# Optimization experiments

Hardware: AMD Instinct MI355X
Metric: run time of the kernel (lower is better)

## Reference

```python
import jax, jax.numpy as jnp
import numpy as np

N_NODES = 65536
N_FEAT = 64
N_EDGES = 1048576
N_GRAPHS = 16
LP_ITERS = 30


def setup_inputs() -> dict:
    key = jax.random.key(0)
    k1, k2, k3 = jax.random.split(key, 3)
    x = jax.random.normal(k1, (N_NODES, N_FEAT), dtype=jnp.float32)
    edge_index = jax.random.randint(k2, (2, N_EDGES), 0, N_NODES, dtype=jnp.int32)
    batch = jnp.sort(jax.random.randint(k3, (N_NODES,), 0, N_GRAPHS, dtype=jnp.int32))
    v2 = jnp.full((1,), 3.5, dtype=jnp.float32)  # learnable affinity scale param
    return {"x": x, "edge_index": edge_index, "batch": batch, "v2": v2}


def _lp_clustering(row, col, aff, n_nodes, n_iters):
    """Label propagation: each node adopts the neighbor label with max summed affinity."""
    E = row.shape[0]
    aff = jax.lax.stop_gradient(aff)  # clustering is discrete, no grad path

    def body(_, labels):
        lab_c = labels[col]                                    # neighbor labels per edge
        order = jnp.lexsort((lab_c, row))                      # sort by (row, neighbor-label)
        r_s, l_s, w_s = row[order], lab_c[order], aff[order]
        new_grp = jnp.concatenate([jnp.ones((1,), bool),
                                   (r_s[1:] != r_s[:-1]) | (l_s[1:] != l_s[:-1])])
        gid = jnp.cumsum(new_grp) - 1                          # dense (row,label) group ids
        gsum = jax.ops.segment_sum(w_s, gid, num_segments=E)   # affinity mass per group
        gcnt = jax.ops.segment_sum(jnp.ones_like(w_s), gid, num_segments=E)
        valid = gcnt > 0
        g_row = jnp.where(valid, jax.ops.segment_max(r_s, gid, num_segments=E), 0)
        g_lab = jnp.where(valid, jax.ops.segment_max(l_s, gid, num_segments=E), n_nodes)
        node_max = jax.ops.segment_max(jnp.where(valid, gsum, -jnp.inf), g_row,
                                       num_segments=n_nodes)
        win = valid & (gsum == node_max[g_row])
        # smallest winning label == torch argmax first-hit tie-break
        return jax.ops.segment_min(jnp.where(win, g_lab, n_nodes), g_row,
                                   num_segments=n_nodes)

    labels0 = jnp.arange(n_nodes, dtype=row.dtype)
    return jax.lax.fori_loop(0, n_iters, body, labels0)


def _forward(x, edge_index, batch, v2):
    n = x.shape[0]
    loops = jnp.arange(n, dtype=edge_index.dtype)
    ei = jnp.concatenate([edge_index, jnp.stack([loops, loops])], axis=1)  # add_self_loops
    row, col = ei[0], ei[1]

    # P2-style affinities: log_aff = -v2 * ||x_i - x_j||^2 ; forward exponentiates
    sqdist = jnp.sum((x[row] - x[col]) ** 2, axis=1)  # [E]
    losses = jnp.mean(sqdist)
    aff = jnp.exp(-v2[0] * sqdist)

    node_labels = _lp_clustering(row, col, aff, n, LP_ITERS)

    # unique(return_inverse): dense relabel of surviving cluster ids (sorted order)
    present = jnp.zeros((n,), jnp.int32).at[node_labels].set(1)
    cluster_labels = (jnp.cumsum(present) - 1)[node_labels]

    # max_pool_x: scatter-max node features into clusters (padded to n rows)
    cx = jax.ops.segment_max(x, cluster_labels, num_segments=n)
    cb = jax.ops.segment_max(batch, cluster_labels, num_segments=n)
    nonempty = jax.ops.segment_sum(jnp.ones((n,), jnp.int32), cluster_labels,
                                   num_segments=n) > 0
    cx = jnp.where(nonempty[:, None], cx, 0.0)
    cb = jnp.where(nonempty, cb, -1)

    # coalesce(cluster_labels[edge_index]): sort + dedupe, duplicates padded with -1
    mr, mc = cluster_labels[row], cluster_labels[col]
    order = jnp.lexsort((mc, mr))
    mr_s, mc_s = mr[order], mc[order]
    dup = jnp.concatenate([jnp.zeros((1,), bool),
                           (mr_s[1:] == mr_s[:-1]) & (mc_s[1:] == mc_s[:-1])])
    cei = jnp.stack([jnp.where(dup, -1, mr_s), jnp.where(dup, -1, mc_s)])

    return cx, cei, cb, cluster_labels, losses


def reference(x, edge_index, batch, v2):
    return _forward(x, edge_index, batch, v2)
```

## Files before the change

### kernel.cpp

```cpp
#include <hip/hip_runtime.h>
#include <hip/hip_fp16.h>
#include <hip/hip_cooperative_groups.h>

namespace cg = cooperative_groups;

#define DI __device__ __forceinline__

constexpr int NN   = 65536;
constexpr int NF   = 64;
constexpr int E0c  = 1048576;
constexpr int ET   = E0c + NN;
constexpr int LPITERS = 30;
constexpr int KPOS = 16;
constexpr int MSCH = 4096;
constexpr int NCHK = ET / MSCH;
constexpr int SCAP = 8192;
constexpr int CAP0 = 6144;
constexpr int EPB  = 128;
constexpr int BPB  = CAP0 / EPB;
constexpr int NPART2 = 256 * BPB;

constexpr int O_CX   = 0;
constexpr int O_CEI0 = NN * NF;
constexpr int O_CEI1 = O_CEI0 + ET;
constexpr int O_CB   = O_CEI0 + 2 * ET;
constexpr int O_CL   = O_CB + NN;
constexpr int O_LOSS = O_CL + NN;

constexpr int W_CHG   = 0;
constexpr int W_NCLUS = 32;
constexpr int W_H1    = 64;
constexpr int W_GC0   = W_H1 + 256;
constexpr int W_GC1   = W_GC0 + 256;
constexpr int W_SCP   = 832;
constexpr int W_SCO   = W_SCP + 256;
constexpr int W_PART  = W_SCO + 256;
constexpr int W_PCNT  = W_PART + NPART2;
constexpr int W_PCOL  = W_PCNT + NN;
constexpr int W_PW    = W_PCOL + NN*KPOS;
constexpr int W_L0    = W_PW + NN*KPOS;
constexpr int W_L1    = W_L0 + NN;
constexpr int W_PRES  = W_L1 + NN;
constexpr int W_PSUM  = W_PRES + NN;
constexpr int W_CLU   = W_PSUM + NN;
constexpr int W_CBA   = W_CLU + NN;
constexpr int W_K0    = W_CBA + NN;
constexpr int W_K1    = W_K0 + 256*CAP0;

DI void edge_rc(const int* ei, int e, int& r, int& c) {
  if (e < E0c) { r = ei[e]; c = ei[E0c + e]; }
  else         { r = e - E0c; c = r; }
}

DI unsigned fenc(float f) {
  unsigned u = __float_as_uint(f);
  return (u & 0x80000000u) ? ~u : (u | 0x80000000u);
}
DI float fdec(unsigned u) {
  u = (u & 0x80000000u) ? (u & 0x7fffffffu) : ~u;
  return __uint_as_float(u);
}

DI int lp_step(int r, int d, int c0, int c1, float q0, float q1,
               const int* __restrict__ pcol, const float* __restrict__ pw,
               const int* __restrict__ lin) {
  int bl = NN;
  if (d == 1) {
    bl = lin[c0];
  } else if (d == 2) {
    int l0 = lin[c0], l1 = lin[c1];
    if (l0 == l1) bl = l0;
    else if (q1 > q0 || (q1 == q0 && l1 < l0)) bl = l1;
    else bl = l0;
  } else if (d > 2) {
    float best = 0.f;
    for (int i = 0; i < d; ++i) {
      int li = lin[pcol[r * KPOS + i]];
      bool dup = false;
      for (int j = 0; j < i; ++j)
        if (lin[pcol[r * KPOS + j]] == li) { dup = true; break; }
      if (dup) continue;
      float sum = 0.f;
      for (int j = i; j < d; ++j)
        if (lin[pcol[r * KPOS + j]] == li) sum += pw[r * KPOS + j];
      if (sum > best || (sum == best && li < bl)) { best = sum; bl = li; }
    }
  }
  return bl;
}


__global__ __launch_bounds__(256) void init_small(int* ws) {
  for (int i = threadIdx.x; i < 832; i += 256) ws[i] = 0;
}

__global__ __launch_bounds__(256) void emultisplit(const int* __restrict__ ei,
                                                   int* __restrict__ gcur0,
                                                   unsigned* __restrict__ K0,
                                                   int* __restrict__ pcnt,
                                                   int* __restrict__ L0,
                                                   const float2* __restrict__ x2,
                                                   unsigned* __restrict__ xh) {
  __shared__ unsigned skey[MSCH];
  __shared__ unsigned short binid[MSCH];
  __shared__ int hl[256], ss[256], hs[256], hc[256], gb[256];
  int t = threadIdx.x;
  if (blockIdx.x < 256) {
    int rr = blockIdx.x * 256 + t;
    pcnt[rr] = 0;
    L0[rr] = rr;
  }
  for (int i = blockIdx.x * 256 + t; i < NN * NF / 2; i += NCHK * 256) {
    float2 f = x2[i];
    __half2 h = __floats2half2_rn(f.x, f.y);
    xh[i] = *reinterpret_cast<unsigned*>(&h);
  }
  hl[t] = 0; __syncthreads();
  int base = blockIdx.x * MSCH;
  unsigned mykey[MSCH / 256];
  #pragma unroll
  for (int k = 0; k < MSCH / 256; ++k) {
    int e = base + k * 256 + t;
    int r, c; edge_rc(ei, e, r, c);
    unsigned key = ((unsigned)r << 16) | (unsigned)c;
    mykey[k] = key;
    atomicAdd(&hl[key >> 24], 1);
  }
  __syncthreads();
  int v = hl[t];
  ss[t] = v; __syncthreads();
  for (int off = 1; off < 256; off <<= 1) {
    int u = (t >= off) ? ss[t - off] : 0;
    __syncthreads();
    ss[t] += u;
    __syncthreads();
  }
  int excl = ss[t] - v;
  hs[t] = excl;
  hc[t] = excl;
  gb[t] = t * CAP0 + ((v > 0) ? atomicAdd(&gcur0[t], v) : 0);
  for (int j = excl; j < excl + v; ++j) binid[j] = (unsigned short)t;
  __syncthreads();
  #pragma unroll
  for (int k = 0; k < MSCH / 256; ++k) {
    int b = mykey[k] >> 24;
    int slot = atomicAdd(&hc[b], 1);
    skey[slot] = mykey[k];
  }
  __syncthreads();
  for (int i = t; i < MSCH; i += 256) {
    int b = binid[i];
    int pos = gb[b] + (i - hs[b]);
    if (pos < (b + 1) * CAP0) K0[pos] = skey[i];
  }
}

__global__ __launch_bounds__(256, 1) void edge_pos2(
    const unsigned* __restrict__ xh, const unsigned* __restrict__ K0,
    const int* __restrict__ gcur0, const float* __restrict__ v2,
    float* __restrict__ part, int* __restrict__ pcnt,
    int* __restrict__ pcol, float* __restrict__ pw) {
  __shared__ float ls[32];
  int t = threadIdx.x, grp = t >> 3, lane = t & 7;
  int bkt = blockIdx.x / BPB;
  int off = (blockIdx.x % BPB) * EPB;
  int cnt = gcur0[bkt];
  if (off >= cnt) {
    if (t == 0) part[blockIdx.x] = 0.f;
    return;
  }
  float w = v2[0];
  unsigned kk[4]; bool act[4];
  uint4 A[4], B[4];
  #pragma unroll
  for (int q = 0; q < 4; ++q) {
    int j = off + grp * 4 + q;
    act[q] = (j < cnt);
    kk[q] = K0[bkt * CAP0 + (act[q] ? j : 0)];
  }
  #pragma unroll
  for (int q = 0; q < 4; ++q) {
    int r = kk[q] >> 16, c = kk[q] & 0xFFFF;
    A[q] = ((const uint4*)(xh + (size_t)r * 32))[lane];
    B[q] = ((const uint4*)(xh + (size_t)c * 32))[lane];
  }
  __builtin_amdgcn_sched_barrier(0);
  float lsum = 0.f;
  #pragma unroll
  for (int q = 0; q < 4; ++q) {
    const __half2* ah = reinterpret_cast<const __half2*>(&A[q]);
    const __half2* bh = reinterpret_cast<const __half2*>(&B[q]);
    __half2 d0 = __hsub2(ah[0], bh[0]);
    __half2 acc = __hmul2(d0, d0);
    __half2 d1 = __hsub2(ah[1], bh[1]); acc = __hfma2(d1, d1, acc);
    __half2 d2 = __hsub2(ah[2], bh[2]); acc = __hfma2(d2, d2, acc);
    __half2 d3 = __hsub2(ah[3], bh[3]); acc = __hfma2(d3, d3, acc);
    float s = __low2float(acc) + __high2float(acc);
    s += __shfl_xor(s, 1, 8);
    s += __shfl_xor(s, 2, 8);
    s += __shfl_xor(s, 4, 8);
    if (lane == 0 && act[q]) {
      int r = kk[q] >> 16, c = kk[q] & 0xFFFF;
      if (r == c) s = 0.f;
      lsum += s;
      float aff = expf(-w * s);
      if (aff > 0.f) {
        int slot = atomicAdd(&pcnt[r], 1);
        if (slot < KPOS) { pcol[r * KPOS + slot] = c; pw[r * KPOS + slot] = aff; }
      }
    }
  }
  if (lane == 0) ls[grp] = lsum;
  __syncthreads();
  if (t == 0) {
    float s = 0.f;
    #pragma unroll
    for (int k = 0; k < 32; ++k) s += ls[k];
    part[blockIdx.x] = s;
  }
}

__global__ __launch_bounds__(256) void lp_iter0(const int* __restrict__ pcnt,
                                                const int* __restrict__ pcol,
                                                const float* __restrict__ pw,
                                                const int* __restrict__ L0,
                                                int* __restrict__ L1,
                                                int* __restrict__ chg,
                                                const float* __restrict__ part,
                                                float* __restrict__ out_loss) {
  __shared__ float smf[256];
  int t = threadIdx.x;
  int r = blockIdx.x * 256 + t;
  int d = pcnt[r];
  if (d > KPOS) d = KPOS;
  int c0 = 0, c1 = 0; float q0 = 0.f, q1 = 0.f;
  if (d >= 1) { c0 = pcol[r * KPOS];     q0 = pw[r * KPOS]; }
  if (d >= 2) { c1 = pcol[r * KPOS + 1]; q1 = pw[r * KPOS + 1]; }
  int bl = lp_step(r, d, c0, c1, q0, q1, pcol, pw, L0);
  L1[r] = bl;
  if (bl != L0[r]) atomicOr(&chg[0], 1);
  if (blockIdx.x == 0) {
    float s = 0.f;
    for (int i = t; i < NPART2; i += 256) s += part[i];
    smf[t] = s; __syncthreads();
    for (int off = 128; off; off >>= 1) {
      if (t < off) smf[t] += smf[t + off];
      __syncthreads();
    }
    if (t == 0) out_loss[0] = smf[0] / (float)ET;
  }
}

__global__ __launch_bounds__(256) void general_tail(
    const int* __restrict__ pcnt, const int* __restrict__ pcol,
    const float* __restrict__ pw, int* __restrict__ L0, int* __restrict__ L1,
    int* __restrict__ chg, int* __restrict__ pres, int* __restrict__ psum,
    int* __restrict__ clu, float* __restrict__ out_cl, int* __restrict__ cba,
    unsigned* __restrict__ cxacc, const float* __restrict__ x,
    const int* __restrict__ batch, int* __restrict__ nclus_g,
    int* __restrict__ scp, int* __restrict__ sco, int* __restrict__ h1,
    const int* __restrict__ gcur0, int* __restrict__ gcur1,
    const unsigned* __restrict__ K0, unsigned* __restrict__ K1,
    float* __restrict__ out_cb) {
  if (chg[0] == 0) return;
  __shared__ int sm[256], hl[256], bases[256];
  __shared__ int sbc;
  cg::grid_group grid = cg::this_grid();
  int t = threadIdx.x, b = blockIdx.x;
  int r = b * 256 + t;
  pres[r] = 0;
  cba[r] = -1;
  {
    uint4 z = make_uint4(0u, 0u, 0u, 0u);
    uint4* p = (uint4*)(cxacc + ((size_t)r << 6));
    #pragma unroll
    for (int q = 0; q < 16; ++q) p[q] = z;
  }
  int mylab = L1[r];
  int d = pcnt[r]; if (d > KPOS) d = KPOS;
  int c0 = 0, c1 = 0; float q0 = 0.f, q1 = 0.f;
  if (d >= 1) { c0 = pcol[r * KPOS];     q0 = pw[r * KPOS]; }
  if (d >= 2) { c1 = pcol[r * KPOS + 1]; q1 = pw[r * KPOS + 1]; }
  for (int it = 1; it < LPITERS; ++it) {
    const int* lin = (it & 1) ? L1 : L0;
    int* lout = (it & 1) ? L0 : L1;
    int bl = lp_step(r, d, c0, c1, q0, q1, pcol, pw, lin);
    lout[r] = bl;
    if (bl != mylab) atomicOr(&chg[it], 1);
    mylab = bl;
    grid.sync();
    if (t == 0) sbc = *(volatile int*)&chg[it];
    __syncthreads();
    if (sbc == 0) break;
  }
  L0[r] = mylab;
  grid.sync();
  pres[mylab] = 1;
  grid.sync();
  int v = pres[r];
  sm[t] = v; __syncthreads();
  for (int off = 1; off < 256; off <<= 1) {
    int u = (t >= off) ? sm[t - off] : 0;
    __syncthreads();
    sm[t] += u;
    __syncthreads();
  }
  int lexcl = sm[t] - v;
  if (t == 255) scp[b] = sm[255];
  grid.sync();
  if (b == 0) {
    int p = scp[t];
    sm[t] = p; __syncthreads();
    for (int off = 1; off < 256; off <<= 1) {
      int u = (t >= off) ? sm[t - off] : 0;
      __syncthreads();
      sm[t] += u;
      __syncthreads();
    }
    sco[t] = sm[t] - p;
    if (t == 255) nclus_g[0] = sm[255];
  }
  grid.sync();
  psum[r] = lexcl + sco[b];
  grid.sync();
  int cr = psum[mylab];
  clu[r] = cr;
  out_cl[r] = (float)cr;
  grid.sync();
  for (int f = 0; f < 64; ++f)
    atomicMax(&cxacc[((size_t)cr << 6) + f], fenc(x[((size_t)r << 6) + f]));
  atomicMax(&cba[cr], batch[r]);
  grid.sync();
  int ncl = nclus_g[0];
  for (int f = 0; f < 64; ++f) {
    unsigned u = cxacc[((size_t)r << 6) + f];
    ((float*)cxacc)[((size_t)r << 6) + f] = (r < ncl) ? fdec(u) : 0.f;
  }
  out_cb[r] = (float)cba[r];
  hl[t] = 0; __syncthreads();
  int cnt = gcur0[b];
  for (int i = t; i < cnt; i += 256) {
    unsigned k = K0[b * CAP0 + i];
    atomicAdd(&hl[((unsigned)clu[k >> 16]) >> 8], 1);
  }
  __syncthreads();
  if (hl[t]) atomicAdd(&h1[t], hl[t]);
  grid.sync();
  int hv = h1[t];
  sm[t] = hv; __syncthreads();
  for (int off = 1; off < 256; off <<= 1) {
    int u = (t >= off) ? sm[t - off] : 0;
    __syncthreads();
    sm[t] += u;
    __syncthreads();
  }
  bases[t] = sm[t] - hv;
  __syncthreads();
  for (int i = t; i < cnt; i += 256) {
    unsigned k = K0[b * CAP0 + i];
    unsigned k1 = ((unsigned)clu[k >> 16] << 16) | (unsigned)clu[k & 0xFFFF];
    int b1 = k1 >> 24;
    int pos = bases[b1] + atomicAdd(&gcur1[b1], 1);
    K1[pos] = k1;
  }
}

__global__ __launch_bounds__(1024) void tail3(
    const unsigned* __restrict__ K0, const int* __restrict__ gcur0,
    unsigned* __restrict__ K1, const int* __restrict__ h1,
    const int* __restrict__ chg, const float4* __restrict__ x4,
    const int* __restrict__ batch, float4* __restrict__ out_cx4,
    float* __restrict__ out_cl, float* __restrict__ out_cb,
    float* __restrict__ o0, float* __restrict__ o1) {
  __shared__ unsigned sk[SCAP];
  __shared__ int hl[256], ss[256], sbs[257], cur[256], sh[2];
  int t = threadIdx.x;
  bool fast = (chg[0] == 0);
  int bb = blockIdx.x;

  if (bb >= 512) {
    if (!fast) return;
    int i = (bb - 512) * 1024 + t;
    out_cx4[i] = x4[i];
    if (i < NN) {
      out_cl[i] = (float)i;
      out_cb[i] = (float)batch[i];
    }
    return;
  }

  if (bb < 256) {
    if (!fast) return;
    int b = bb;
    int cntb = gcur0[b];
    if (cntb > CAP0) cntb = CAP0;
    if (t < 256) ss[t] = gcur0[t];
    __syncthreads();
    for (int off = 1; off < 256; off <<= 1) {
      int u = (t < 256 && t >= off) ? ss[t - off] : 0;
      __syncthreads();
      if (t < 256) ss[t] += u;
      __syncthreads();
    }
    if (t == 0) sh[0] = ss[b] - gcur0[b];
    if (t < 256) hl[t] = 0;
    __syncthreads();
    for (int i = t; i < cntb; i += 1024)
      atomicAdd(&hl[(K0[b * CAP0 + i] >> 16) & 0xFF], 1);
    __syncthreads();
    if (t < 256) ss[t] = hl[t];
    __syncthreads();
    for (int off = 1; off < 256; off <<= 1) {
      int u = (t < 256 && t >= off) ? ss[t - off] : 0;
      __syncthreads();
      if (t < 256) ss[t] += u;
      __syncthreads();
    }
    if (t < 256) { sbs[t] = ss[t] - hl[t]; cur[t] = ss[t] - hl[t]; }
    if (t == 255) sbs[256] = cntb;
    __syncthreads();
    for (int i = t; i < cntb; i += 1024) {
      unsigned k = K0[b * CAP0 + i];
      int slot = atomicAdd(&cur[(k >> 16) & 0xFF], 1);
      sk[slot] = k;
    }
    __syncthreads();
    int wave = t >> 6, lane = t & 63;
    for (int sb = wave; sb < 256; sb += 16) {
      int s0 = sbs[sb], s1 = sbs[sb + 1], dd = s1 - s0;
      if (dd <= 1) continue;
      if (dd <= 64) {
        unsigned k = (lane < dd) ? sk[s0 + lane] : 0xFFFFFFFFu;
        int P = (dd <= 16) ? 16 : ((dd <= 32) ? 32 : 64);
        for (int size = 2; size <= P; size <<= 1) {
          bool upAll = (size == P);
          for (int stride = size >> 1; stride > 0; stride >>= 1) {
            unsigned o = __shfl_xor(k, stride, 64);
            bool up = upAll || ((lane & size) == 0);
            bool takeMin = (((lane & stride) == 0) == up);
            unsigned mn = k < o ? k : o, mx = k < o ? o : k;
            k = takeMin ? mn : mx;
          }
        }
        if (lane < dd) sk[s0 + lane] = k;
      } else if (lane == 0) {
        for (int i = s0 + 1; i < s1; ++i) {
          unsigned k = sk[i];
          int j = i - 1;
          while (j >= s0 && sk[j] > k) { sk[j + 1] = sk[j]; --j; }
          sk[j + 1] = k;
        }
      }
    }
    __syncthreads();
    int sout = sh[0];
    for (int i = t; i < cntb; i += 1024) {
      unsigned k = sk[i];
      bool dup = (i > 0) && (sk[i - 1] == k);
      o0[sout + i] = dup ? -1.f : (float)(k >> 16);
      o1[sout + i] = dup ? -1.f : (float)(k & 0xffffu);
    }
    return;
  }

  if (fast) return;
  int b = bb - 256;
  if (t < 256) ss[t] = h1[t];
  __syncthreads();
  for (int off = 1; off < 256; off <<= 1) {
    int u = (t < 256 && t >= off) ? ss[t - off] : 0;
    __syncthreads();
    if (t < 256) ss[t] += u;
    __syncthreads();
  }
  if (t == 0) { sh[0] = ss[b] - h1[b]; sh[1] = h1[b]; }
  __syncthreads();
  int sout = sh[0], d = sh[1];
  if (d <= 0) return;
  unsigned* kp = K1 + sout;
  if (d <= SCAP) {
    if (t < 256) hl[t] = 0;
    __syncthreads();
    for (int i = t; i < d; i += 1024)
      atomicAdd(&hl[(kp[i] >> 16) & 0xFF], 1);
    __syncthreads();
    if (t < 256) ss[t] = hl[t];
    __syncthreads();
    for (int off = 1; off < 256; off <<= 1) {
      int u = (t < 256 && t >= off) ? ss[t - off] : 0;
      __syncthreads();
      if (t < 256) ss[t] += u;
      __syncthreads();
    }
    if (t < 256) { sbs[t] = ss[t] - hl[t]; cur[t] = ss[t] - hl[t]; }
    if (t == 255) sbs[256] = d;
    __syncthreads();
    for (int i = t; i < d; i += 1024) {
      unsigned k = kp[i];
      int slot = atomicAdd(&cur[(k >> 16) & 0xFF], 1);
      sk[slot] = k;
    }
    __syncthreads();
    int wave = t >> 6, lane = t & 63;
    for (int sb = wave; sb < 256; sb += 16) {
      int s0 = sbs[sb], s1 = sbs[sb + 1], dd = s1 - s0;
      if (dd <= 1) continue;
      if (dd <= 64) {
        unsigned k = (lane < dd) ? sk[s0 + lane] : 0xFFFFFFFFu;
        #pragma unroll
        for (int size = 2; size <= 64; size <<= 1) {
          #pragma unroll
          for (int stride = size >> 1; stride > 0; stride >>= 1) {
            unsigned o = __shfl_xor(k, stride, 64);
            bool takeMin = (((lane & stride) == 0) == ((lane & size) == 0));
            unsigned mn = k < o ? k : o, mx = k < o ? o : k;
            k = takeMin ? mn : mx;
          }
        }
        if (lane < dd) sk[s0 + lane] = k;
      } else if (lane == 0) {
        for (int i = s0 + 1; i < s1; ++i) {
          unsigned k = sk[i];
          int j = i - 1;
          while (j >= s0 && sk[j] > k) { sk[j + 1] = sk[j]; --j; }
          sk[j + 1] = k;
        }
      }
    }
    __syncthreads();
    for (int i = t; i < d; i += 1024) {
      unsigned k = sk[i];
      bool dup = (i > 0) && (sk[i - 1] == k);
      o0[sout + i] = dup ? -1.f : (float)(k >> 16);
      o1[sout + i] = dup ? -1.f : (float)(k & 0xffffu);
    }
  } else {
    if (t == 0) {
      for (int i = 1; i < d; ++i) {
        unsigned k = kp[i];
        int j = i - 1;
        while (j >= 0 && kp[j] > k) { kp[j + 1] = kp[j]; --j; }
        kp[j + 1] = k;
      }
    }
    __syncthreads();
    for (int i = t; i < d; i += 1024) {
      unsigned k = kp[i];
      bool dup = (i > 0) && (kp[i - 1] == k);
      o0[sout + i] = dup ? -1.f : (float)(k >> 16);
      o1[sout + i] = dup ? -1.f : (float)(k & 0xffffu);
    }
  }
}


extern "C" void kernel_launch(void* const* d_in, const int* in_sizes, int n_in,
                              void* d_out, int out_size, void* d_ws, size_t ws_size,
                              hipStream_t stream) {
  const float* x   = (const float*)d_in[0];
  const int* ei    = (const int*)d_in[1];
  const int* batch = (const int*)d_in[2];
  const float* v2  = (const float*)d_in[3];
  float* out = (float*)d_out;
  int* ws = (int*)d_ws;
  unsigned* cxacc = (unsigned*)(out + O_CX);
  unsigned* xh = cxacc;

  init_small<<<1, 256, 0, stream>>>(ws);

  emultisplit<<<NCHK, 256, 0, stream>>>(ei, ws + W_GC0, (unsigned*)(ws + W_K0),
                                        ws + W_PCNT, ws + W_L0,
                                        (const float2*)x, xh);

  edge_pos2<<<NPART2, 256, 0, stream>>>(xh, (const unsigned*)(ws + W_K0),
                                        ws + W_GC0, v2, (float*)(ws + W_PART),
                                        ws + W_PCNT, ws + W_PCOL, (float*)(ws + W_PW));

  lp_iter0<<<NN / 256, 256, 0, stream>>>(ws + W_PCNT, ws + W_PCOL,
                                         (const float*)(ws + W_PW),
                                         ws + W_L0, ws + W_L1, ws + W_CHG,
                                         (const float*)(ws + W_PART), out + O_LOSS);

  {
    const int* pcnt = ws + W_PCNT;
    const int* pcol = ws + W_PCOL;
    const float* pw = (const float*)(ws + W_PW);
    int* L0 = ws + W_L0;
    int* L1 = ws + W_L1;
    int* chg = ws + W_CHG;
    int* pres = ws + W_PRES;
    int* psum = ws + W_PSUM;
    int* clu = ws + W_CLU;
    float* out_cl = out + O_CL;
    int* cba = ws + W_CBA;
    unsigned* cxa = cxacc;
    const float* x_ = x;
    const int* batch_ = batch;
    int* nclus_g = ws + W_NCLUS;
    int* scp = ws + W_SCP;
    int* sco = ws + W_SCO;
    int* h1 = ws + W_H1;
    const int* gcur0 = ws + W_GC0;
    int* gcur1 = ws + W_GC1;
    const unsigned* K0 = (const unsigned*)(ws + W_K0);
    unsigned* K1 = (unsigned*)(ws + W_K1);
    float* out_cb = out + O_CB;
    void* args[] = { (void*)&pcnt, (void*)&pcol, (void*)&pw,
                     (void*)&L0, (void*)&L1, (void*)&chg, (void*)&pres,
                     (void*)&psum, (void*)&clu, (void*)&out_cl, (void*)&cba,
                     (void*)&cxa, (void*)&x_, (void*)&batch_, (void*)&nclus_g,
                     (void*)&scp, (void*)&sco, (void*)&h1, (void*)&gcur0,
                     (void*)&gcur1, (void*)&K0, (void*)&K1, (void*)&out_cb };
    hipLaunchCooperativeKernel((const void*)general_tail, dim3(NN / 256),
                               dim3(256), args, 0, stream);
  }

  tail3<<<1536, 1024, 0, stream>>>((const unsigned*)(ws + W_K0), ws + W_GC0,
                                   (unsigned*)(ws + W_K1), ws + W_H1,
                                   ws + W_CHG, (const float4*)x, batch,
                                   (float4*)(out + O_CX), out + O_CL,
                                   out + O_CB, out + O_CEI0, out + O_CEI1);
}
```

Measured before the change: 137.4 us.

## Split edge buckets into 1024 finer bins and shrink tail3 blocks to 256 threads

Edge keys are now multisplit into 1024 buckets by the top 10 bits of the row instead of 256 by the top 8, with per-bucket capacity cut to 1536. The prefix offsets of the buckets are computed once in lp_iter0 and stored in workspace, so tail3 no longer recomputes a 256-wide scan in every block. tail3 runs as 2304 blocks of 256 threads, each sorting a smaller bucket with 64 sub-bins, which is meant to raise parallelism and occupancy in the final coalesce sort. The cost is more global atomics and more bins per chunk in emultisplit, plus a higher chance that a bucket overflows its fixed capacity.

```diff
diff --git a/kernel.cpp b/kernel.cpp
--- a/kernel.cpp
+++ b/kernel.cpp
@@ -15,10 +15,11 @@
 constexpr int MSCH = 4096;
 constexpr int NCHK = ET / MSCH;
 constexpr int SCAP = 8192;
-constexpr int CAP0 = 6144;
+constexpr int NB   = 1024;
+constexpr int CAPB = 1536;
 constexpr int EPB  = 128;
-constexpr int BPB  = CAP0 / EPB;
-constexpr int NPART2 = 256 * BPB;
+constexpr int BPB  = CAPB / EPB;
+constexpr int NPART2 = NB * BPB;
 
 constexpr int O_CX   = 0;
 constexpr int O_CEI0 = NN * NF;
@@ -30,9 +31,10 @@
 constexpr int W_CHG   = 0;
 constexpr int W_NCLUS = 32;
 constexpr int W_H1    = 64;
-constexpr int W_GC0   = W_H1 + 256;
-constexpr int W_GC1   = W_GC0 + 256;
-constexpr int W_SCP   = 832;
+constexpr int W_GC0   = 320;
+constexpr int W_GC1   = 1344;
+constexpr int W_GB    = 1600;
+constexpr int W_SCP   = W_GB + 1024;
 constexpr int W_SCO   = W_SCP + 256;
 constexpr int W_PART  = W_SCO + 256;
 constexpr int W_PCNT  = W_PART + NPART2;
@@ -45,7 +47,7 @@
 constexpr int W_CLU   = W_PSUM + NN;
 constexpr int W_CBA   = W_CLU + NN;
 constexpr int W_K0    = W_CBA + NN;
-constexpr int W_K1    = W_K0 + 256*CAP0;
+constexpr int W_K1    = W_K0 + NB*CAPB;
 
 DI void edge_rc(const int* ei, int e, int& r, int& c) {
   if (e < E0c) { r = ei[e]; c = ei[E0c + e]; }
@@ -91,7 +93,7 @@
 
 
 __global__ __launch_bounds__(256) void init_small(int* ws) {
-  for (int i = threadIdx.x; i < 832; i += 256) ws[i] = 0;
+  for (int i = threadIdx.x; i < 1600; i += 256) ws[i] = 0;
 }
 
 __global__ __launch_bounds__(256) void emultisplit(const int* __restrict__ ei,
@@ -103,7 +105,7 @@
                                                    unsigned* __restrict__ xh) {
   __shared__ unsigned skey[MSCH];
   __shared__ unsigned short binid[MSCH];
-  __shared__ int hl[256], ss[256], hs[256], hc[256], gb[256];
+  __shared__ int hl[NB], hs[NB], hc[NB], gb[NB], s4[256];
   int t = threadIdx.x;
   if (blockIdx.x < 256) {
     int rr = blockIdx.x * 256 + t;
@@ -115,7 +117,9 @@
     __half2 h = __floats2half2_rn(f.x, f.y);
     xh[i] = *reinterpret_cast<unsigned*>(&h);
   }
-  hl[t] = 0; __syncthreads();
+  #pragma unroll
+  for (int q = 0; q < 4; ++q) hl[t * 4 + q] = 0;
+  __syncthreads();
   int base = blockIdx.x * MSCH;
   unsigned mykey[MSCH / 256];
   #pragma unroll
@@ -124,26 +128,33 @@
     int r, c; edge_rc(ei, e, r, c);
     unsigned key = ((unsigned)r << 16) | (unsigned)c;
     mykey[k] = key;
-    atomicAdd(&hl[key >> 24], 1);
-  }
-  __syncthreads();
-  int v = hl[t];
-  ss[t] = v; __syncthreads();
+    atomicAdd(&hl[key >> 22], 1);
+  }
+  __syncthreads();
+  int v0 = hl[t * 4], v1 = hl[t * 4 + 1], v2 = hl[t * 4 + 2], v3 = hl[t * 4 + 3];
+  int msum = v0 + v1 + v2 + v3;
+  s4[t] = msum; __syncthreads();
   for (int off = 1; off < 256; off <<= 1) {
-    int u = (t >= off) ? ss[t - off] : 0;
-    __syncthreads();
-    ss[t] += u;
-    __syncthreads();
-  }
-  int excl = ss[t] - v;
-  hs[t] = excl;
-  hc[t] = excl;
-  gb[t] = t * CAP0 + ((v > 0) ? atomicAdd(&gcur0[t], v) : 0);
-  for (int j = excl; j < excl + v; ++j) binid[j] = (unsigned short)t;
+    int u = (t >= off) ? s4[t - off] : 0;
+    __syncthreads();
+    s4[t] += u;
+    __syncthreads();
+  }
+  int e0 = s4[t] - msum, e1 = e0 + v0, e2 = e1 + v1, e3 = e2 + v2;
+  hs[t*4] = e0; hs[t*4+1] = e1; hs[t*4+2] = e2; hs[t*4+3] = e3;
+  hc[t*4] = e0; hc[t*4+1] = e1; hc[t*4+2] = e2; hc[t*4+3] = e3;
+  gb[t*4]   = (t*4)   * CAPB + ((v0 > 0) ? atomicAdd(&gcur0[t*4],   v0) : 0);
+  gb[t*4+1] = (t*4+1) * CAPB + ((v1 > 0) ? atomicAdd(&gcur0[t*4+1], v1) : 0);
+  gb[t*4+2] = (t*4+2) * CAPB + ((v2 > 0) ? atomicAdd(&gcur0[t*4+2], v2) : 0);
+  gb[t*4+3] = (t*4+3) * CAPB + ((v3 > 0) ? atomicAdd(&gcur0[t*4+3], v3) : 0);
+  for (int j = e0; j < e1; ++j) binid[j] = (unsigned short)(t*4);
+  for (int j = e1; j < e2; ++j) binid[j] = (unsigned short)(t*4+1);
+  for (int j = e2; j < e3; ++j) binid[j] = (unsigned short)(t*4+2);
+  for (int j = e3; j < e3 + v3; ++j) binid[j] = (unsigned short)(t*4+3);
   __syncthreads();
   #pragma unroll
   for (int k = 0; k < MSCH / 256; ++k) {
-    int b = mykey[k] >> 24;
+    int b = mykey[k] >> 22;
     int slot = atomicAdd(&hc[b], 1);
     skey[slot] = mykey[k];
   }
@@ -151,7 +162,7 @@
   for (int i = t; i < MSCH; i += 256) {
     int b = binid[i];
     int pos = gb[b] + (i - hs[b]);
-    if (pos < (b + 1) * CAP0) K0[pos] = skey[i];
+    if (pos < (b + 1) * CAPB) K0[pos] = skey[i];
   }
 }
 
@@ -176,7 +187,7 @@
   for (int q = 0; q < 4; ++q) {
     int j = off + grp * 4 + q;
     act[q] = (j < cnt);
-    kk[q] = K0[bkt * CAP0 + (act[q] ? j : 0)];
+    kk[q] = K0[bkt * CAPB + (act[q] ? j : 0)];
   }
   #pragma unroll
   for (int q = 0; q < 4; ++q) {
@@ -227,8 +238,11 @@
                                                 int* __restrict__ L1,
                                                 int* __restrict__ chg,
                                                 const float* __restrict__ part,
-                                                float* __restrict__ out_loss) {
+                                                float* __restrict__ out_loss,
+                                                const int* __restrict__ gcur0,
+                                                int* __restrict__ gbase) {
   __shared__ float smf[256];
+  __shared__ int s4[256];
   int t = threadIdx.x;
   int r = blockIdx.x * 256 + t;
   int d = pcnt[r];
@@ -248,6 +262,19 @@
       __syncthreads();
     }
     if (t == 0) out_loss[0] = smf[0] / (float)ET;
+  } else if (blockIdx.x == 1) {
+    int v0 = gcur0[t*4], v1 = gcur0[t*4+1], v2 = gcur0[t*4+2], v3 = gcur0[t*4+3];
+    int msum = v0 + v1 + v2 + v3;
+    s4[t] = msum; __syncthreads();
+    for (int off = 1; off < 256; off <<= 1) {
+      int u = (t >= off) ? s4[t - off] : 0;
+      __syncthreads();
+      s4[t] += u;
+      __syncthreads();
+    }
+    int e0 = s4[t] - msum;
+    gbase[t*4] = e0; gbase[t*4+1] = e0 + v0;
+    gbase[t*4+2] = e0 + v0 + v1; gbase[t*4+3] = e0 + v0 + v1 + v2;
   }
 }
 
@@ -338,10 +365,13 @@
   }
   out_cb[r] = (float)cba[r];
   hl[t] = 0; __syncthreads();
-  int cnt = gcur0[b];
-  for (int i = t; i < cnt; i += 256) {
-    unsigned k = K0[b * CAP0 + i];
-    atomicAdd(&hl[((unsigned)clu[k >> 16]) >> 8], 1);
+  for (int sub = 0; sub < 4; ++sub) {
+    int bkt = b * 4 + sub;
+    int cnt = gcur0[bkt];
+    for (int i = t; i < cnt; i += 256) {
+      unsigned k = K0[bkt * CAPB + i];
+      atomicAdd(&hl[((unsigned)clu[k >> 16]) >> 8], 1);
+    }
   }
   __syncthreads();
   if (hl[t]) atomicAdd(&h1[t], hl[t]);
@@ -356,32 +386,39 @@
   }
   bases[t] = sm[t] - hv;
   __syncthreads();
-  for (int i = t; i < cnt; i += 256) {
-    unsigned k = K0[b * CAP0 + i];
-    unsigned k1 = ((unsigned)clu[k >> 16] << 16) | (unsigned)clu[k & 0xFFFF];
-    int b1 = k1 >> 24;
-    int pos = bases[b1] + atomicAdd(&gcur1[b1], 1);
-    K1[pos] = k1;
-  }
-}
-
-__global__ __launch_bounds__(1024) void tail3(
+  for (int sub = 0; sub < 4; ++sub) {
+    int bkt = b * 4 + sub;
+    int cnt = gcur0[bkt];
+    for (int i = t; i < cnt; i += 256) {
+      unsigned k = K0[bkt * CAPB + i];
+      unsigned k1 = ((unsigned)clu[k >> 16] << 16) | (unsigned)clu[k & 0xFFFF];
+      int b1 = k1 >> 24;
+      int pos = bases[b1] + atomicAdd(&gcur1[b1], 1);
+      K1[pos] = k1;
+    }
+  }
+}
+
+__global__ __launch_bounds__(256) void tail3(
     const unsigned* __restrict__ K0, const int* __restrict__ gcur0,
-    unsigned* __restrict__ K1, const int* __restrict__ h1,
-    const int* __restrict__ chg, const float4* __restrict__ x4,
-    const int* __restrict__ batch, float4* __restrict__ out_cx4,
-    float* __restrict__ out_cl, float* __restrict__ out_cb,
-    float* __restrict__ o0, float* __restrict__ o1) {
+    const int* __restrict__ gbase, unsigned* __restrict__ K1,
+    const int* __restrict__ h1, const int* __restrict__ chg,
+    const float4* __restrict__ x4, const int* __restrict__ batch,
+    float4* __restrict__ out_cx4, float* __restrict__ out_cl,
+    float* __restrict__ out_cb, float* __restrict__ o0,
+    float* __restrict__ o1) {
   __shared__ unsigned sk[SCAP];
   __shared__ int hl[256], ss[256], sbs[257], cur[256], sh[2];
   int t = threadIdx.x;
   bool fast = (chg[0] == 0);
   int bb = blockIdx.x;
 
-  if (bb >= 512) {
+  if (bb >= 1280) {
     if (!fast) return;
-    int i = (bb - 512) * 1024 + t;
-    out_cx4[i] = x4[i];
+    int base = (bb - 1280) * 1024 + t;
+    #pragma unroll
+    for (int k = 0; k < 4; ++k) out_cx4[base + k * 256] = x4[base + k * 256];
+    int i = (bb - 1280) * 256 + t;
     if (i < NN) {
       out_cl[i] = (float)i;
       out_cb[i] = (float)batch[i];
@@ -389,44 +426,37 @@
     return;
   }
 
-  if (bb < 256) {
+  if (bb < 1024) {
     if (!fast) return;
     int b = bb;
     int cntb = gcur0[b];
-    if (cntb > CAP0) cntb = CAP0;
-    if (t < 256) ss[t] = gcur0[t];
-    __syncthreads();
-    for (int off = 1; off < 256; off <<= 1) {
-      int u = (t < 256 && t >= off) ? ss[t - off] : 0;
-      __syncthreads();
-      if (t < 256) ss[t] += u;
-      __syncthreads();
-    }
-    if (t == 0) sh[0] = ss[b] - gcur0[b];
-    if (t < 256) hl[t] = 0;
-    __syncthreads();
-    for (int i = t; i < cntb; i += 1024)
-      atomicAdd(&hl[(K0[b * CAP0 + i] >> 16) & 0xFF], 1);
-    __syncthreads();
-    if (t < 256) ss[t] = hl[t];
-    __syncthreads();
-    for (int off = 1; off < 256; off <<= 1) {
-      int u = (t < 256 && t >= off) ? ss[t - off] : 0;
-      __syncthreads();
-      if (t < 256) ss[t] += u;
-      __syncthreads();
-    }
-    if (t < 256) { sbs[t] = ss[t] - hl[t]; cur[t] = ss[t] - hl[t]; }
-    if (t == 255) sbs[256] = cntb;
-    __syncthreads();
-    for (int i = t; i < cntb; i += 1024) {
-      unsigned k = K0[b * CAP0 + i];
-      int slot = atomicAdd(&cur[(k >> 16) & 0xFF], 1);
+    if (cntb > CAPB) cntb = CAPB;
+    if (cntb <= 0) return;
+    int sout = gbase[b];
+    if (t < 64) { hl[t] = 0; }
+    __syncthreads();
+    for (int i = t; i < cntb; i += 256)
+      atomicAdd(&hl[(K0[b * CAPB + i] >> 16) & 63], 1);
+    __syncthreads();
+    if (t < 64) ss[t] = hl[t];
+    __syncthreads();
+    for (int off = 1; off < 64; off <<= 1) {
+      int u = (t < 64 && t >= off) ? ss[t - off] : 0;
+      __syncthreads();
+      if (t < 64) ss[t] += u;
+      __syncthreads();
+    }
+    if (t < 64) { sbs[t] = ss[t] - hl[t]; cur[t] = ss[t] - hl[t]; }
+    if (t == 63) sbs[64] = cntb;
+    __syncthreads();
+    for (int i = t; i < cntb; i += 256) {
+      unsigned k = K0[b * CAPB + i];
+      int slot = atomicAdd(&cur[(k >> 16) & 63], 1);
       sk[slot] = k;
     }
     __syncthreads();
     int wave = t >> 6, lane = t & 63;
-    for (int sb = wave; sb < 256; sb += 16) {
+    for (int sb = wave; sb < 64; sb += 4) {
       int s0 = sbs[sb], s1 = sbs[sb + 1], dd = s1 - s0;
       if (dd <= 1) continue;
       if (dd <= 64) {
@@ -453,8 +483,7 @@
       }
     }
     __syncthreads();
-    int sout = sh[0];
-    for (int i = t; i < cntb; i += 1024) {
+    for (int i = t; i < cntb; i += 256) {
       unsigned k = sk[i];
       bool dup = (i > 0) && (sk[i - 1] == k);
       o0[sout + i] = dup ? -1.f : (float)(k >> 16);
@@ -464,13 +493,13 @@
   }
 
   if (fast) return;
-  int b = bb - 256;
+  int b = bb - 1024;
   if (t < 256) ss[t] = h1[t];
   __syncthreads();
   for (int off = 1; off < 256; off <<= 1) {
-    int u = (t < 256 && t >= off) ? ss[t - off] : 0;
-    __syncthreads();
-    if (t < 256) ss[t] += u;
+    int u = (t >= off) ? ss[t - off] : 0;
+    __syncthreads();
+    ss[t] += u;
     __syncthreads();
   }
   if (t == 0) { sh[0] = ss[b] - h1[b]; sh[1] = h1[b]; }
@@ -479,30 +508,30 @@
   if (d <= 0) return;
   unsigned* kp = K1 + sout;
   if (d <= SCAP) {
-    if (t < 256) hl[t] = 0;
-    __syncthreads();
-    for (int i = t; i < d; i += 1024)
+    hl[t] = 0;
+    __syncthreads();
+    for (int i = t; i < d; i += 256)
       atomicAdd(&hl[(kp[i] >> 16) & 0xFF], 1);
     __syncthreads();
-    if (t < 256) ss[t] = hl[t];
+    ss[t] = hl[t];
     __syncthreads();
     for (int off = 1; off < 256; off <<= 1) {
-      int u = (t < 256 && t >= off) ? ss[t - off] : 0;
-      __syncthreads();
-      if (t < 256) ss[t] += u;
-      __syncthreads();
-    }
-    if (t < 256) { sbs[t] = ss[t] - hl[t]; cur[t] = ss[t] - hl[t]; }
+      int u = (t >= off) ? ss[t - off] : 0;
+      __syncthreads();
+      ss[t] += u;
+      __syncthreads();
+    }
+    sbs[t] = ss[t] - hl[t]; cur[t] = ss[t] - hl[t];
     if (t == 255) sbs[256] = d;
     __syncthreads();
-    for (int i = t; i < d; i += 1024) {
+    for (int i = t; i < d; i += 256) {
       unsigned k = kp[i];
       int slot = atomicAdd(&cur[(k >> 16) & 0xFF], 1);
       sk[slot] = k;
     }
     __syncthreads();
     int wave = t >> 6, lane = t & 63;
-    for (int sb = wave; sb < 256; sb += 16) {
+    for (int sb = wave; sb < 256; sb += 4) {
       int s0 = sbs[sb], s1 = sbs[sb + 1], dd = s1 - s0;
       if (dd <= 1) continue;
       if (dd <= 64) {
@@ -528,7 +557,7 @@
       }
     }
     __syncthreads();
-    for (int i = t; i < d; i += 1024) {
+    for (int i = t; i < d; i += 256) {
       unsigned k = sk[i];
       bool dup = (i > 0) && (sk[i - 1] == k);
       o0[sout + i] = dup ? -1.f : (float)(k >> 16);
@@ -544,7 +573,7 @@
       }
     }
     __syncthreads();
-    for (int i = t; i < d; i += 1024) {
+    for (int i = t; i < d; i += 256) {
       unsigned k = kp[i];
       bool dup = (i > 0) && (kp[i - 1] == k);
       o0[sout + i] = dup ? -1.f : (float)(k >> 16);
@@ -579,7 +608,8 @@
   lp_iter0<<<NN / 256, 256, 0, stream>>>(ws + W_PCNT, ws + W_PCOL,
                                          (const float*)(ws + W_PW),
                                          ws + W_L0, ws + W_L1, ws + W_CHG,
-                                         (const float*)(ws + W_PART), out + O_LOSS);
+                                         (const float*)(ws + W_PART), out + O_LOSS,
+                                         ws + W_GC0, ws + W_GB);
 
   {
     const int* pcnt = ws + W_PCNT;
@@ -615,9 +645,9 @@
                                dim3(256), args, 0, stream);
   }
 
-  tail3<<<1536, 1024, 0, stream>>>((const unsigned*)(ws + W_K0), ws + W_GC0,
-                                   (unsigned*)(ws + W_K1), ws + W_H1,
-                                   ws + W_CHG, (const float4*)x, batch,
-                                   (float4*)(out + O_CX), out + O_CL,
-                                   out + O_CB, out + O_CEI0, out + O_CEI1);
-}
+  tail3<<<2304, 256, 0, stream>>>((const unsigned*)(ws + W_K0), ws + W_GC0,
+                                  ws + W_GB, (unsigned*)(ws + W_K1), ws + W_H1,
+                                  ws + W_CHG, (const float4*)x, batch,
+                                  (float4*)(out + O_CX), out + O_CL,
+                                  out + O_CB, out + O_CEI0, out + O_CEI1);
+}
```

Measured after the change: 149.1 us. 1.08x slower.
